# Optimization experiments

Measured on AMD Instinct MI355X. Metric: run time of the kernel, lower is better.

Reference implementation:

```python
import jax, jax.numpy as jnp
import numpy as np
import math

B, T, C, H = 2, 2048, 1024, 16
D = C // H  # head dim = 64
ROPE_BASE = 10000.0


def _rope(x):
    # x: (B, T, H, D); interleaved-pair RoPE matching torch apply_rope
    theta = jnp.exp(jnp.arange(0, D, 2, dtype=jnp.float32) * (-math.log(ROPE_BASE) / D))  # (D/2,)
    ang = jnp.arange(T, dtype=jnp.float32)[:, None] * theta[None, :]  # (T, D/2)
    cos = jnp.cos(ang)[None, :, None, :]  # (1, T, 1, D/2)
    sin = jnp.sin(ang)[None, :, None, :]
    xr = x.reshape(B, T, H, D // 2, 2)
    x0, x1 = xr[..., 0], xr[..., 1]
    out = jnp.stack([x0 * cos - x1 * sin, x1 * cos + x0 * sin], axis=-1)
    return out.reshape(B, T, H, D).astype(x.dtype)


def setup_inputs() -> dict:
    key = jax.random.key(0)
    k0, k1, k2 = jax.random.split(key, 3)
    x = jax.random.normal(k0, (B, T, C), dtype=jnp.float32)
    Wqkv = jax.random.normal(k1, (3 * C, C), dtype=jnp.float32) * 0.02
    bqkv = jnp.zeros((3 * C,), dtype=jnp.float32)
    Wproj = jax.random.normal(k2, (C, C), dtype=jnp.float32) * 0.02
    bproj = jnp.zeros((C,), dtype=jnp.float32)
    return {"x": x, "Wqkv": Wqkv, "bqkv": bqkv, "Wproj": Wproj, "bproj": bproj}


def reference(x, Wqkv, bqkv, Wproj, bproj):
    qkv = x @ Wqkv.T + bqkv  # (B, T, 3C)
    q, k, v = jnp.split(qkv, 3, axis=-1)
    q = _rope(q.reshape(B, T, H, D)).transpose(0, 2, 1, 3)  # (B, H, T, D)
    k = _rope(k.reshape(B, T, H, D)).transpose(0, 2, 1, 3)
    v = v.reshape(B, T, H, D).transpose(0, 2, 1, 3)
    scores = jnp.einsum('bhqd,bhkd->bhqk', q, k) * (1.0 / math.sqrt(D))
    causal = jnp.tril(jnp.ones((T, T), dtype=bool))  # (T, T)
    scores = jnp.where(causal[None, None, :, :], scores, -jnp.inf)
    attn = jax.nn.softmax(scores, axis=-1)
    y = jnp.einsum('bhqk,bhkd->bhqd', attn, v)  # (B, H, T, D)
    y = y.transpose(0, 2, 1, 3).reshape(B, T, C)
    return y @ Wproj.T + bproj
```

## Files before the change

kernel.cpp:

```cpp
#include <hip/hip_runtime.h>

typedef unsigned short u16;
typedef unsigned int u32;
typedef __bf16 bf16x8 __attribute__((ext_vector_type(8)));
typedef float f32x4 __attribute__((ext_vector_type(4)));
typedef float f32x16 __attribute__((ext_vector_type(16)));

#define BB 2
#define TT 2048
#define CC 1024
#define HH 16
#define DD 64
#define MR (BB*TT)
#define NQ (3*CC)

__device__ __forceinline__ u16 f2b(float f) {
    u32 u = __builtin_bit_cast(u32, f);
    u = (u + 0x7fffu + ((u >> 16) & 1u)) >> 16;
    return (u16)u;
}
__device__ __forceinline__ float b2f(u16 b) {
    return __builtin_bit_cast(float, (u32)b << 16);
}
__device__ __forceinline__ u32 pkbf(float a, float b) {
    ushort2 t; t.x = f2b(a); t.y = f2b(b);
    return __builtin_bit_cast(u32, t);
}

__device__ __forceinline__ void gll16(const void* g, void* l) {
    __builtin_amdgcn_global_load_lds(
        (const __attribute__((address_space(1))) void*)g,
        (__attribute__((address_space(3))) void*)l,
        16, 0, 0);
}

__global__ void cvt_all(const float* __restrict__ x, const float* __restrict__ wqkv,
                        const float* __restrict__ wproj,
                        u16* __restrict__ xb, u16* __restrict__ wqkvb, u16* __restrict__ wprojb)
{
    const int n0 = MR * CC / 4, n1 = NQ * CC / 4, n2 = CC * CC / 4;
    int i = blockIdx.x * 256 + threadIdx.x;
    const float* src; u16* dst; int off;
    if (i < n0)           { src = x;     dst = xb;     off = i; }
    else if (i < n0 + n1) { src = wqkv;  dst = wqkvb;  off = i - n0; }
    else if (i < n0 + n1 + n2) { src = wproj; dst = wprojb; off = i - n0 - n1; }
    else return;
    float4 v = reinterpret_cast<const float4*>(src)[off];
    ushort4 o;
    o.x = f2b(v.x); o.y = f2b(v.y); o.z = f2b(v.z); o.w = f2b(v.w);
    reinterpret_cast<ushort4*>(dst)[off] = o;
}

template<int BF16_OUT>
__global__ __launch_bounds__(256) void gemm_bt(
    const u16* __restrict__ A, const u16* __restrict__ Bm,
    const float* __restrict__ bias, void* __restrict__ outp,
    int M, int N, int K)
{
    __shared__ __align__(16) u16 As[128 * 32];
    __shared__ __align__(16) u16 Bs[128 * 32];
    const int tid = threadIdx.x;
    const int lane = tid & 63;
    const int w = tid >> 6;
    const int wr = w >> 1, wc = w & 1;
    const int fr = lane & 15, fq = lane >> 4;
    const int brow = blockIdx.y * 128, bcol = blockIdx.x * 128;
    const int srow = lane >> 2;
    const int scol = (lane & 3) * 8;

    f32x4 acc[4][4];
    const f32x4 zero = {0.f, 0.f, 0.f, 0.f};
#pragma unroll
    for (int i = 0; i < 4; i++)
#pragma unroll
        for (int j = 0; j < 4; j++) acc[i][j] = zero;

    for (int kt = 0; kt < K; kt += 32) {
#pragma unroll
        for (int i = 0; i < 2; i++) {
            const int r = i * 64 + w * 16 + srow;
            gll16(&A[(size_t)(brow + r) * K + kt + scol], &As[(i * 64 + w * 16) * 32]);
            gll16(&Bm[(size_t)(bcol + r) * K + kt + scol], &Bs[(i * 64 + w * 16) * 32]);
        }
        __syncthreads();
        bf16x8 af[4], bfr[4];
#pragma unroll
        for (int mi = 0; mi < 4; mi++)
            af[mi] = *reinterpret_cast<const bf16x8*>(&As[(wr * 64 + mi * 16 + fr) * 32 + fq * 8]);
#pragma unroll
        for (int nj = 0; nj < 4; nj++)
            bfr[nj] = *reinterpret_cast<const bf16x8*>(&Bs[(wc * 64 + nj * 16 + fr) * 32 + fq * 8]);
#pragma unroll
        for (int mi = 0; mi < 4; mi++)
#pragma unroll
            for (int nj = 0; nj < 4; nj++)
                acc[mi][nj] = __builtin_amdgcn_mfma_f32_16x16x32_bf16(af[mi], bfr[nj], acc[mi][nj], 0, 0, 0);
        __syncthreads();
    }

#pragma unroll
    for (int mi = 0; mi < 4; mi++) {
#pragma unroll
        for (int nj = 0; nj < 4; nj++) {
            const int n = bcol + wc * 64 + nj * 16 + fr;
            const float bn = bias[n];
#pragma unroll
            for (int r = 0; r < 4; r++) {
                const int m = brow + wr * 64 + mi * 16 + fq * 4 + r;
                const float v = acc[mi][nj][r] + bn;
                if (BF16_OUT) reinterpret_cast<u16*>(outp)[(size_t)m * N + n] = f2b(v);
                else          reinterpret_cast<float*>(outp)[(size_t)m * N + n] = v;
            }
        }
    }
}

__global__ void rope_reorder(const u16* __restrict__ qkv,
                             u16* __restrict__ Qr, u16* __restrict__ Kr)
{
    const int idx = blockIdx.x * 256 + threadIdx.x;
    const int j = idx & 31;
    const int h = (idx >> 5) & 15;
    const int t = (idx >> 9) & 2047;
    const int b = idx >> 20;
    const size_t mrow = (size_t)(b * TT + t) * NQ;
    const float theta = __expf((float)(2 * j) * (-0.14391157f));
    const float ang = (float)t * theta;
    const float cs = cosf(ang), sn = sinf(ang);
    const int qc = h * DD + 2 * j;
    const float q0 = b2f(qkv[mrow + qc]),          q1 = b2f(qkv[mrow + qc + 1]);
    const float k0 = b2f(qkv[mrow + CC + qc]),     k1 = b2f(qkv[mrow + CC + qc + 1]);
    const size_t obase = ((size_t)(b * HH + h) * TT + t) * DD + 2 * j;
    Qr[obase]     = f2b(q0 * cs - q1 * sn);
    Qr[obase + 1] = f2b(q1 * cs + q0 * sn);
    Kr[obase]     = f2b(k0 * cs - k1 * sn);
    Kr[obase + 1] = f2b(k1 * cs + k0 * sn);
}

__global__ __launch_bounds__(64) void vtrans(const u16* __restrict__ qkv, u16* __restrict__ Vtg)
{
    const int lane = threadIdx.x;
    const int t0 = blockIdx.x * 64;
    const int bh = blockIdx.y;
    const int b = bh >> 4, h = bh & 15;
    u32 packed[32];
#pragma unroll
    for (int tt = 0; tt < 64; tt += 2) {
        const u16 a = qkv[(size_t)(b * TT + t0 + tt) * NQ + 2 * CC + h * DD + lane];
        const u16 c = qkv[(size_t)(b * TT + t0 + tt + 1) * NQ + 2 * CC + h * DD + lane];
        packed[tt >> 1] = (u32)a | ((u32)c << 16);
    }
    u32* dst = reinterpret_cast<u32*>(&Vtg[((size_t)bh * DD + lane) * TT + t0]);
#pragma unroll
    for (int i = 0; i < 32; i += 4)
        *reinterpret_cast<uint4*>(&dst[i]) = make_uint4(packed[i], packed[i + 1], packed[i + 2], packed[i + 3]);
}

__global__ __launch_bounds__(256) void attn_fwd(
    const u16* __restrict__ Q, const u16* __restrict__ Kg, const u16* __restrict__ Vtg,
    u16* __restrict__ Y)
{
    __shared__ __align__(16) u16 smem[64 * 72 * 2];
    u16* Ks = smem;
    u16* Vs = smem + 64 * 72;

    const int tid = threadIdx.x;
    const int lane = tid & 63, w = tid >> 6;
    const int ql = lane & 31;
    const int hB = lane >> 5;
    const int id = blockIdx.x;
    const int xcd = id & 7, l = id >> 3;
    const int bh = (l & 3) * 8 + xcd;
    const int bx = (l < 32) ? (15 - (l >> 2)) : ((l - 32) >> 2);
    const int q0 = bx * 128;
    const int b = bh >> 4, hh = bh & 15;
    const int qb = q0 + w * 32;
    const int qg = qb + ql;
    const size_t base = (size_t)bh * TT * DD;
    const size_t vbase = (size_t)bh * DD * TT;

    bf16x8 qf[4];
#pragma unroll
    for (int ds = 0; ds < 4; ds++)
        qf[ds] = *reinterpret_cast<const bf16x8*>(&Q[base + (size_t)qg * DD + ds * 16 + hB * 8]);

    f32x16 acc[2];
#pragma unroll
    for (int dh = 0; dh < 2; dh++)
#pragma unroll
        for (int r = 0; r < 16; r++) acc[dh][r] = 0.f;
    float m_ = -1e30f, l_ = 0.f;

    const int srow = tid >> 2;
    const int sc = tid & 3;

    const int kv_end = q0 + 128;
    for (int kv0 = 0; kv0 < kv_end; kv0 += 64) {
#pragma unroll
        for (int rr = 0; rr < 2; rr++) {
            const int cu = (rr * 4 + sc) * 8;
            *reinterpret_cast<uint4*>(&Ks[srow * 72 + cu]) =
                *reinterpret_cast<const uint4*>(&Kg[base + (size_t)(kv0 + srow) * DD + cu]);
            *reinterpret_cast<uint4*>(&Vs[srow * 72 + cu]) =
                *reinterpret_cast<const uint4*>(&Vtg[vbase + (size_t)srow * TT + kv0 + cu]);
        }
        __syncthreads();

        if (kv0 <= qb + 31) {
            f32x16 sa[2];
#pragma unroll
            for (int st = 0; st < 2; st++)
#pragma unroll
                for (int r = 0; r < 16; r++) sa[st][r] = 0.f;
            __builtin_amdgcn_s_setprio(1);
#pragma unroll
            for (int st = 0; st < 2; st++)
#pragma unroll
                for (int ds = 0; ds < 4; ds++) {
                    bf16x8 kf = *reinterpret_cast<const bf16x8*>(
                        &Ks[(st * 32 + ql) * 72 + ds * 16 + hB * 8]);
                    sa[st] = __builtin_amdgcn_mfma_f32_32x32x16_bf16(kf, qf[ds], sa[st], 0, 0, 0);
                }
            __builtin_amdgcn_s_setprio(0);
#pragma unroll
            for (int st = 0; st < 2; st++) {
                const int kb0 = kv0 + st * 32 + 4 * hB;
#pragma unroll
                for (int r = 0; r < 16; r++) {
                    const int kg = kb0 + (r & 3) + 8 * (r >> 2);
                    const float v = sa[st][r] * 0.125f;
                    sa[st][r] = (kg > qg) ? -1e30f : v;
                }
            }
            float tm = sa[0][0];
#pragma unroll
            for (int r = 1; r < 16; r++) tm = fmaxf(tm, sa[0][r]);
#pragma unroll
            for (int r = 0; r < 16; r++) tm = fmaxf(tm, sa[1][r]);
            tm = fmaxf(tm, __shfl_xor(tm, 32));
            const float mn = fmaxf(m_, tm);
            const float scl = __expf(m_ - mn);
            m_ = mn;
            float rs = 0.f;
#pragma unroll
            for (int st = 0; st < 2; st++)
#pragma unroll
                for (int r = 0; r < 16; r++) {
                    const float p = __expf(sa[st][r] - mn);
                    sa[st][r] = p;
                    rs += p;
                }
            rs += __shfl_xor(rs, 32);
            l_ = l_ * scl + rs;
#pragma unroll
            for (int dh = 0; dh < 2; dh++)
#pragma unroll
                for (int r = 0; r < 16; r++) acc[dh][r] *= scl;
            u32 pk[2][8];
#pragma unroll
            for (int st = 0; st < 2; st++)
#pragma unroll
                for (int wd = 0; wd < 8; wd++)
                    pk[st][wd] = pkbf(sa[st][2 * wd], sa[st][2 * wd + 1]);
            __builtin_amdgcn_s_setprio(1);
#pragma unroll
            for (int c = 0; c < 4; c++) {
                u32 a0 = pk[c >> 1][4 * (c & 1) + 0];
                u32 a1 = pk[c >> 1][4 * (c & 1) + 1];
                u32 a2 = pk[c >> 1][4 * (c & 1) + 2];
                u32 a3 = pk[c >> 1][4 * (c & 1) + 3];
                asm volatile("v_permlane32_swap_b32 %0, %1" : "+v"(a0), "+v"(a2));
                asm volatile("v_permlane32_swap_b32 %0, %1" : "+v"(a1), "+v"(a3));
                uint4 tw = make_uint4(a0, a1, a2, a3);
                bf16x8 pb = __builtin_bit_cast(bf16x8, tw);
#pragma unroll
                for (int dh = 0; dh < 2; dh++) {
                    bf16x8 vf = *reinterpret_cast<const bf16x8*>(
                        &Vs[(dh * 32 + ql) * 72 + c * 16 + hB * 8]);
                    acc[dh] = __builtin_amdgcn_mfma_f32_32x32x16_bf16(vf, pb, acc[dh], 0, 0, 0);
                }
            }
            __builtin_amdgcn_s_setprio(0);
        }
        __syncthreads();
    }

    const float linv = 1.0f / l_;
    u16* sw = smem + w * (32 * 72);
#pragma unroll
    for (int dh = 0; dh < 2; dh++)
#pragma unroll
        for (int rp = 0; rp < 16; rp += 2) {
            const int d = (rp & 3) + 8 * (rp >> 2) + 4 * hB + 32 * dh;
            *reinterpret_cast<u32*>(&sw[ql * 72 + d]) =
                pkbf(acc[dh][rp] * linv, acc[dh][rp + 1] * linv);
        }
    const int orow = lane >> 1, ocol = (lane & 1) * 32;
    const size_t ybase = (size_t)(b * TT + qb + orow) * CC + hh * DD + ocol;
#pragma unroll
    for (int i = 0; i < 4; i++) {
        uint4 ov = *reinterpret_cast<const uint4*>(&sw[orow * 72 + ocol + i * 8]);
        *reinterpret_cast<uint4*>(&Y[ybase + i * 8]) = ov;
    }
}

extern "C" void kernel_launch(void* const* d_in, const int* in_sizes, int n_in,
                              void* d_out, int out_size, void* d_ws, size_t ws_size,
                              hipStream_t stream)
{
    const float* x     = (const float*)d_in[0];
    const float* Wqkv  = (const float*)d_in[1];
    const float* bqkv  = (const float*)d_in[2];
    const float* Wproj = (const float*)d_in[3];
    const float* bproj = (const float*)d_in[4];
    float* out = (float*)d_out;

    u16* ws     = (u16*)d_ws;
    u16* xb     = ws;
    u16* wqkvb  = xb     + (size_t)MR * CC;
    u16* wprojb = wqkvb  + (size_t)NQ * CC;
    u16* qkv    = wprojb + (size_t)CC * CC;
    u16* Qr     = qkv    + (size_t)MR * NQ;
    u16* Kr     = Qr     + (size_t)BB * HH * TT * DD;
    u16* Vtg    = Kr     + (size_t)BB * HH * TT * DD;
    u16* yb     = Vtg    + (size_t)BB * HH * TT * DD;

    cvt_all<<<dim3(8192), 256, 0, stream>>>(x, Wqkv, Wproj, xb, wqkvb, wprojb);

    gemm_bt<1><<<dim3(NQ / 128, MR / 128), 256, 0, stream>>>(xb, wqkvb, bqkv, qkv, MR, NQ, CC);

    rope_reorder<<<dim3(BB * TT * HH * 32 / 256), 256, 0, stream>>>(qkv, Qr, Kr);
    vtrans<<<dim3(TT / 64, BB * HH), 64, 0, stream>>>(qkv, Vtg);

    attn_fwd<<<dim3(512), 256, 0, stream>>>(Qr, Kr, Vtg, yb);

    gemm_bt<0><<<dim3(CC / 128, MR / 128), 256, 0, stream>>>(yb, wprojb, bproj, out, MR, CC, CC);
}
```

Before: 228.7 us.

## Split KV range across two warp groups with persistent atomic work queue

The attention kernel becomes persistent: 256 blocks of 512 threads pull (q-tile, head) items from a global atomic counter, which is reset inside the conversion kernel. Each block holds two warp groups that process alternating 64-key tiles and merge their partial softmax states through shared memory. K/V loads are register-prefetched one tile ahead. The softmax scale and log2(e) are folded into Q during RoPE so exp2f can be used, masking runs only on diagonal tiles, and accumulator rescaling is skipped when the running max does not change. The cost is extra merge traffic and barriers per item, plus dependence on the counter reset ordering.

```diff
diff --git a/kernel.cpp b/kernel.cpp
--- a/kernel.cpp
+++ b/kernel.cpp
@@ -13,6 +13,7 @@
 #define DD 64
 #define MR (BB*TT)
 #define NQ (3*CC)
+#define SCQ 0.18033688f
 
 __device__ __forceinline__ u16 f2b(float f) {
     u32 u = __builtin_bit_cast(u32, f);
@@ -36,8 +37,10 @@
 
 __global__ void cvt_all(const float* __restrict__ x, const float* __restrict__ wqkv,
                         const float* __restrict__ wproj,
-                        u16* __restrict__ xb, u16* __restrict__ wqkvb, u16* __restrict__ wprojb)
-{
+                        u16* __restrict__ xb, u16* __restrict__ wqkvb, u16* __restrict__ wprojb,
+                        u32* __restrict__ ctr)
+{
+    if (blockIdx.x == 0 && threadIdx.x == 0) *ctr = 0;
     const int n0 = MR * CC / 4, n1 = NQ * CC / 4, n2 = CC * CC / 4;
     int i = blockIdx.x * 256 + threadIdx.x;
     const float* src; u16* dst; int off;
@@ -131,8 +134,8 @@
     const float q0 = b2f(qkv[mrow + qc]),          q1 = b2f(qkv[mrow + qc + 1]);
     const float k0 = b2f(qkv[mrow + CC + qc]),     k1 = b2f(qkv[mrow + CC + qc + 1]);
     const size_t obase = ((size_t)(b * HH + h) * TT + t) * DD + 2 * j;
-    Qr[obase]     = f2b(q0 * cs - q1 * sn);
-    Qr[obase + 1] = f2b(q1 * cs + q0 * sn);
+    Qr[obase]     = f2b((q0 * cs - q1 * sn) * SCQ);
+    Qr[obase + 1] = f2b((q1 * cs + q0 * sn) * SCQ);
     Kr[obase]     = f2b(k0 * cs - k1 * sn);
     Kr[obase + 1] = f2b(k1 * cs + k0 * sn);
 }
@@ -156,151 +159,221 @@
         *reinterpret_cast<uint4*>(&dst[i]) = make_uint4(packed[i], packed[i + 1], packed[i + 2], packed[i + 3]);
 }
 
-__global__ __launch_bounds__(256) void attn_fwd(
+__global__ __launch_bounds__(512) void attn_fwd(
     const u16* __restrict__ Q, const u16* __restrict__ Kg, const u16* __restrict__ Vtg,
-    u16* __restrict__ Y)
-{
-    __shared__ __align__(16) u16 smem[64 * 72 * 2];
-    u16* Ks = smem;
-    u16* Vs = smem + 64 * 72;
-
+    u16* __restrict__ Y, u32* __restrict__ ctr)
+{
+    __shared__ __align__(16) u16 smem[4 * 64 * 72];
+    __shared__ int cur;
     const int tid = threadIdx.x;
-    const int lane = tid & 63, w = tid >> 6;
+    const int lane = tid & 63;
     const int ql = lane & 31;
     const int hB = lane >> 5;
-    const int id = blockIdx.x;
-    const int xcd = id & 7, l = id >> 3;
-    const int bh = (l & 3) * 8 + xcd;
-    const int bx = (l < 32) ? (15 - (l >> 2)) : ((l - 32) >> 2);
-    const int q0 = bx * 128;
-    const int b = bh >> 4, hh = bh & 15;
-    const int qb = q0 + w * 32;
-    const int qg = qb + ql;
-    const size_t base = (size_t)bh * TT * DD;
-    const size_t vbase = (size_t)bh * DD * TT;
-
-    bf16x8 qf[4];
-#pragma unroll
-    for (int ds = 0; ds < 4; ds++)
-        qf[ds] = *reinterpret_cast<const bf16x8*>(&Q[base + (size_t)qg * DD + ds * 16 + hB * 8]);
-
-    f32x16 acc[2];
-#pragma unroll
-    for (int dh = 0; dh < 2; dh++)
-#pragma unroll
-        for (int r = 0; r < 16; r++) acc[dh][r] = 0.f;
-    float m_ = -1e30f, l_ = 0.f;
-
-    const int srow = tid >> 2;
-    const int sc = tid & 3;
-
-    const int kv_end = q0 + 128;
-    for (int kv0 = 0; kv0 < kv_end; kv0 += 64) {
-#pragma unroll
-        for (int rr = 0; rr < 2; rr++) {
-            const int cu = (rr * 4 + sc) * 8;
-            *reinterpret_cast<uint4*>(&Ks[srow * 72 + cu]) =
-                *reinterpret_cast<const uint4*>(&Kg[base + (size_t)(kv0 + srow) * DD + cu]);
-            *reinterpret_cast<uint4*>(&Vs[srow * 72 + cu]) =
-                *reinterpret_cast<const uint4*>(&Vtg[vbase + (size_t)srow * TT + kv0 + cu]);
-        }
-        __syncthreads();
-
-        if (kv0 <= qb + 31) {
-            f32x16 sa[2];
-#pragma unroll
-            for (int st = 0; st < 2; st++)
-#pragma unroll
-                for (int r = 0; r < 16; r++) sa[st][r] = 0.f;
-            __builtin_amdgcn_s_setprio(1);
-#pragma unroll
-            for (int st = 0; st < 2; st++)
-#pragma unroll
-                for (int ds = 0; ds < 4; ds++) {
-                    bf16x8 kf = *reinterpret_cast<const bf16x8*>(
-                        &Ks[(st * 32 + ql) * 72 + ds * 16 + hB * 8]);
-                    sa[st] = __builtin_amdgcn_mfma_f32_32x32x16_bf16(kf, qf[ds], sa[st], 0, 0, 0);
+    const int wq = (tid >> 6) & 3;
+    const int g  = tid >> 8;
+    const int srow = (tid & 255) >> 2;
+    const int sc   = tid & 3;
+    u16* KsG = smem + (g * 2 + 0) * 4608;
+    u16* VsG = smem + (g * 2 + 1) * 4608;
+    float* fm = reinterpret_cast<float*>(smem);
+
+    while (true) {
+        if (tid == 0) cur = atomicAdd(ctr, 1);
+        __syncthreads();
+        const int it = cur;
+        __syncthreads();
+        if (it >= 512) break;
+
+        const int bx = 15 - (it >> 5);
+        const int bh = it & 31;
+        const int q0 = bx << 7;
+        const int halfL = bx + 1;
+        const int b = bh >> 4, hh = bh & 15;
+        const int qb = q0 + wq * 32;
+        const int qg = qb + ql;
+        const size_t base  = (size_t)bh * TT * DD;
+        const size_t vbase = (size_t)bh * DD * TT;
+
+        bf16x8 qf[4];
+#pragma unroll
+        for (int ds = 0; ds < 4; ds++)
+            qf[ds] = *reinterpret_cast<const bf16x8*>(&Q[base + (size_t)qg * DD + ds * 16 + hB * 8]);
+
+        f32x16 acc[2];
+#pragma unroll
+        for (int dh = 0; dh < 2; dh++)
+#pragma unroll
+            for (int r = 0; r < 16; r++) acc[dh][r] = 0.f;
+        float m_ = -1e30f, l_ = 0.f;
+
+        int kv0 = 64 * g;
+        uint4 kr0, kr1, vr0, vr1;
+        {
+            const size_t kro = base + (size_t)(kv0 + srow) * DD;
+            kr0 = *reinterpret_cast<const uint4*>(&Kg[kro + sc * 8]);
+            kr1 = *reinterpret_cast<const uint4*>(&Kg[kro + 32 + sc * 8]);
+            const size_t vro = vbase + (size_t)srow * TT + kv0;
+            vr0 = *reinterpret_cast<const uint4*>(&Vtg[vro + sc * 8]);
+            vr1 = *reinterpret_cast<const uint4*>(&Vtg[vro + 32 + sc * 8]);
+        }
+
+        for (int i = 0; i < halfL; ++i) {
+            *reinterpret_cast<uint4*>(&KsG[srow * 72 + sc * 8])      = kr0;
+            *reinterpret_cast<uint4*>(&KsG[srow * 72 + 32 + sc * 8]) = kr1;
+            *reinterpret_cast<uint4*>(&VsG[srow * 72 + sc * 8])      = vr0;
+            *reinterpret_cast<uint4*>(&VsG[srow * 72 + 32 + sc * 8]) = vr1;
+            if (i + 1 < halfL) {
+                const size_t kro = base + (size_t)(kv0 + 128 + srow) * DD;
+                kr0 = *reinterpret_cast<const uint4*>(&Kg[kro + sc * 8]);
+                kr1 = *reinterpret_cast<const uint4*>(&Kg[kro + 32 + sc * 8]);
+                const size_t vro = vbase + (size_t)srow * TT + kv0 + 128;
+                vr0 = *reinterpret_cast<const uint4*>(&Vtg[vro + sc * 8]);
+                vr1 = *reinterpret_cast<const uint4*>(&Vtg[vro + 32 + sc * 8]);
+            }
+            __syncthreads();
+
+            if (kv0 <= qb + 31) {
+                f32x16 sa[2];
+#pragma unroll
+                for (int st = 0; st < 2; st++)
+#pragma unroll
+                    for (int r = 0; r < 16; r++) sa[st][r] = 0.f;
+                __builtin_amdgcn_s_setprio(1);
+#pragma unroll
+                for (int st = 0; st < 2; st++)
+#pragma unroll
+                    for (int ds = 0; ds < 4; ds++) {
+                        bf16x8 kf = *reinterpret_cast<const bf16x8*>(
+                            &KsG[(st * 32 + ql) * 72 + ds * 16 + hB * 8]);
+                        sa[st] = __builtin_amdgcn_mfma_f32_32x32x16_bf16(kf, qf[ds], sa[st], 0, 0, 0);
+                    }
+                __builtin_amdgcn_s_setprio(0);
+                if (kv0 + 63 > qb) {
+#pragma unroll
+                    for (int st = 0; st < 2; st++) {
+                        const int kb0 = kv0 + st * 32 + 4 * hB;
+#pragma unroll
+                        for (int r = 0; r < 16; r++) {
+                            const int kg = kb0 + (r & 3) + 8 * (r >> 2);
+                            if (kg > qg) sa[st][r] = -1e30f;
+                        }
+                    }
                 }
-            __builtin_amdgcn_s_setprio(0);
-#pragma unroll
-            for (int st = 0; st < 2; st++) {
-                const int kb0 = kv0 + st * 32 + 4 * hB;
-#pragma unroll
-                for (int r = 0; r < 16; r++) {
-                    const int kg = kb0 + (r & 3) + 8 * (r >> 2);
-                    const float v = sa[st][r] * 0.125f;
-                    sa[st][r] = (kg > qg) ? -1e30f : v;
+                float mx[16];
+#pragma unroll
+                for (int j = 0; j < 16; j++) mx[j] = fmaxf(sa[0][j], sa[1][j]);
+#pragma unroll
+                for (int j = 0; j < 8; j++) mx[j] = fmaxf(mx[j], mx[j + 8]);
+#pragma unroll
+                for (int j = 0; j < 4; j++) mx[j] = fmaxf(mx[j], mx[j + 4]);
+                float tm = fmaxf(fmaxf(mx[0], mx[1]), fmaxf(mx[2], mx[3]));
+                tm = fmaxf(tm, __shfl_xor(tm, 32));
+                const float mn = fmaxf(m_, tm);
+                const bool need = __any(mn > m_);
+                float scl = 1.0f;
+                if (need) { scl = exp2f(m_ - mn); m_ = mn; }
+#pragma unroll
+                for (int st = 0; st < 2; st++)
+#pragma unroll
+                    for (int r = 0; r < 16; r++)
+                        sa[st][r] = exp2f(sa[st][r] - m_);
+                float ps[16];
+#pragma unroll
+                for (int j = 0; j < 16; j++) ps[j] = sa[0][j] + sa[1][j];
+#pragma unroll
+                for (int j = 0; j < 8; j++) ps[j] += ps[j + 8];
+#pragma unroll
+                for (int j = 0; j < 4; j++) ps[j] += ps[j + 4];
+                float rs = (ps[0] + ps[1]) + (ps[2] + ps[3]);
+                rs += __shfl_xor(rs, 32);
+                if (need) {
+                    l_ = l_ * scl + rs;
+#pragma unroll
+                    for (int dh = 0; dh < 2; dh++)
+#pragma unroll
+                        for (int r = 0; r < 16; r++) acc[dh][r] *= scl;
+                } else {
+                    l_ += rs;
                 }
+                u32 pk[2][8];
+#pragma unroll
+                for (int st = 0; st < 2; st++)
+#pragma unroll
+                    for (int wd = 0; wd < 8; wd++)
+                        pk[st][wd] = pkbf(sa[st][2 * wd], sa[st][2 * wd + 1]);
+                __builtin_amdgcn_s_setprio(1);
+#pragma unroll
+                for (int c = 0; c < 4; c++) {
+                    u32 a0 = pk[c >> 1][4 * (c & 1) + 0];
+                    u32 a1 = pk[c >> 1][4 * (c & 1) + 1];
+                    u32 a2 = pk[c >> 1][4 * (c & 1) + 2];
+                    u32 a3 = pk[c >> 1][4 * (c & 1) + 3];
+                    asm volatile("v_permlane32_swap_b32 %0, %1" : "+v"(a0), "+v"(a2));
+                    asm volatile("v_permlane32_swap_b32 %0, %1" : "+v"(a1), "+v"(a3));
+                    uint4 tw = make_uint4(a0, a1, a2, a3);
+                    bf16x8 pb = __builtin_bit_cast(bf16x8, tw);
+#pragma unroll
+                    for (int dh = 0; dh < 2; dh++) {
+                        bf16x8 vf = *reinterpret_cast<const bf16x8*>(
+                            &VsG[(dh * 32 + ql) * 72 + c * 16 + hB * 8]);
+                        acc[dh] = __builtin_amdgcn_mfma_f32_32x32x16_bf16(vf, pb, acc[dh], 0, 0, 0);
+                    }
+                }
+                __builtin_amdgcn_s_setprio(0);
             }
-            float tm = sa[0][0];
-#pragma unroll
-            for (int r = 1; r < 16; r++) tm = fmaxf(tm, sa[0][r]);
-#pragma unroll
-            for (int r = 0; r < 16; r++) tm = fmaxf(tm, sa[1][r]);
-            tm = fmaxf(tm, __shfl_xor(tm, 32));
-            const float mn = fmaxf(m_, tm);
-            const float scl = __expf(m_ - mn);
-            m_ = mn;
-            float rs = 0.f;
-#pragma unroll
-            for (int st = 0; st < 2; st++)
-#pragma unroll
-                for (int r = 0; r < 16; r++) {
-                    const float p = __expf(sa[st][r] - mn);
-                    sa[st][r] = p;
-                    rs += p;
+            __syncthreads();
+            kv0 += 128;
+        }
+
+        const int fidx = (wq * 64 + lane) * 36;
+        if (g == 1) {
+#pragma unroll
+            for (int dh = 0; dh < 2; dh++)
+#pragma unroll
+                for (int r = 0; r < 16; r++) fm[fidx + dh * 16 + r] = acc[dh][r];
+            fm[fidx + 32] = m_;
+            fm[fidx + 33] = l_;
+        }
+        __syncthreads();
+        float o_sc1 = 0.f, o_sc2 = 0.f, linv = 0.f;
+        float acc2[32];
+        if (g == 0) {
+            const float m2 = fm[fidx + 32];
+            const float l2 = fm[fidx + 33];
+            const float mm = fmaxf(m_, m2);
+            o_sc1 = exp2f(m_ - mm);
+            o_sc2 = exp2f(m2 - mm);
+            const float lt = l_ * o_sc1 + l2 * o_sc2;
+            linv = 1.0f / lt;
+#pragma unroll
+            for (int dh = 0; dh < 2; dh++)
+#pragma unroll
+                for (int r = 0; r < 16; r++) acc2[dh * 16 + r] = fm[fidx + dh * 16 + r];
+        }
+        __syncthreads();
+        if (g == 0) {
+            const int lrow = wq * 32 + ql;
+#pragma unroll
+            for (int dh = 0; dh < 2; dh++)
+#pragma unroll
+                for (int rp = 0; rp < 16; rp += 2) {
+                    const int d = (rp & 3) + 8 * (rp >> 2) + 4 * hB + 32 * dh;
+                    const float v0 = (acc[dh][rp]     * o_sc1 + acc2[dh * 16 + rp]     * o_sc2) * linv;
+                    const float v1 = (acc[dh][rp + 1] * o_sc1 + acc2[dh * 16 + rp + 1] * o_sc2) * linv;
+                    *reinterpret_cast<u32*>(&smem[lrow * 72 + d]) = pkbf(v0, v1);
                 }
-            rs += __shfl_xor(rs, 32);
-            l_ = l_ * scl + rs;
-#pragma unroll
-            for (int dh = 0; dh < 2; dh++)
-#pragma unroll
-                for (int r = 0; r < 16; r++) acc[dh][r] *= scl;
-            u32 pk[2][8];
-#pragma unroll
-            for (int st = 0; st < 2; st++)
-#pragma unroll
-                for (int wd = 0; wd < 8; wd++)
-                    pk[st][wd] = pkbf(sa[st][2 * wd], sa[st][2 * wd + 1]);
-            __builtin_amdgcn_s_setprio(1);
-#pragma unroll
-            for (int c = 0; c < 4; c++) {
-                u32 a0 = pk[c >> 1][4 * (c & 1) + 0];
-                u32 a1 = pk[c >> 1][4 * (c & 1) + 1];
-                u32 a2 = pk[c >> 1][4 * (c & 1) + 2];
-                u32 a3 = pk[c >> 1][4 * (c & 1) + 3];
-                asm volatile("v_permlane32_swap_b32 %0, %1" : "+v"(a0), "+v"(a2));
-                asm volatile("v_permlane32_swap_b32 %0, %1" : "+v"(a1), "+v"(a3));
-                uint4 tw = make_uint4(a0, a1, a2, a3);
-                bf16x8 pb = __builtin_bit_cast(bf16x8, tw);
-#pragma unroll
-                for (int dh = 0; dh < 2; dh++) {
-                    bf16x8 vf = *reinterpret_cast<const bf16x8*>(
-                        &Vs[(dh * 32 + ql) * 72 + c * 16 + hB * 8]);
-                    acc[dh] = __builtin_amdgcn_mfma_f32_32x32x16_bf16(vf, pb, acc[dh], 0, 0, 0);
-                }
+        }
+        __syncthreads();
+        {
+            const int row = tid >> 2;
+            const int ch = tid & 3;
+#pragma unroll
+            for (int p = 0; p < 2; ++p) {
+                uint4 ov = *reinterpret_cast<const uint4*>(&smem[row * 72 + (ch + 4 * p) * 8]);
+                *reinterpret_cast<uint4*>(&Y[(size_t)(b * TT + q0 + row) * CC + hh * DD + (ch + 4 * p) * 8]) = ov;
             }
-            __builtin_amdgcn_s_setprio(0);
-        }
-        __syncthreads();
-    }
-
-    const float linv = 1.0f / l_;
-    u16* sw = smem + w * (32 * 72);
-#pragma unroll
-    for (int dh = 0; dh < 2; dh++)
-#pragma unroll
-        for (int rp = 0; rp < 16; rp += 2) {
-            const int d = (rp & 3) + 8 * (rp >> 2) + 4 * hB + 32 * dh;
-            *reinterpret_cast<u32*>(&sw[ql * 72 + d]) =
-                pkbf(acc[dh][rp] * linv, acc[dh][rp + 1] * linv);
-        }
-    const int orow = lane >> 1, ocol = (lane & 1) * 32;
-    const size_t ybase = (size_t)(b * TT + qb + orow) * CC + hh * DD + ocol;
-#pragma unroll
-    for (int i = 0; i < 4; i++) {
-        uint4 ov = *reinterpret_cast<const uint4*>(&sw[orow * 72 + ocol + i * 8]);
-        *reinterpret_cast<uint4*>(&Y[ybase + i * 8]) = ov;
+        }
+        __syncthreads();
     }
 }
 
@@ -324,15 +397,16 @@
     u16* Kr     = Qr     + (size_t)BB * HH * TT * DD;
     u16* Vtg    = Kr     + (size_t)BB * HH * TT * DD;
     u16* yb     = Vtg    + (size_t)BB * HH * TT * DD;
-
-    cvt_all<<<dim3(8192), 256, 0, stream>>>(x, Wqkv, Wproj, xb, wqkvb, wprojb);
+    u32* ctr    = (u32*)(yb + (size_t)MR * CC);
+
+    cvt_all<<<dim3(8192), 256, 0, stream>>>(x, Wqkv, Wproj, xb, wqkvb, wprojb, ctr);
 
     gemm_bt<1><<<dim3(NQ / 128, MR / 128), 256, 0, stream>>>(xb, wqkvb, bqkv, qkv, MR, NQ, CC);
 
     rope_reorder<<<dim3(BB * TT * HH * 32 / 256), 256, 0, stream>>>(qkv, Qr, Kr);
     vtrans<<<dim3(TT / 64, BB * HH), 64, 0, stream>>>(qkv, Vtg);
 
-    attn_fwd<<<dim3(512), 256, 0, stream>>>(Qr, Kr, Vtg, yb);
+    attn_fwd<<<dim3(256), 512, 0, stream>>>(Qr, Kr, Vtg, yb, ctr);
 
     gemm_bt<0><<<dim3(CC / 128, MR / 128), 256, 0, stream>>>(yb, wprojb, bproj, out, MR, CC, CC);
 }
```

Result: faster. 217.7 us (-4.8%).
